# Kernel optimization log

Hardware: AMD Instinct MI355X
Metric: run time of the kernel (lower is better)

The kernel has to match this reference:

```python
import jax, jax.numpy as jnp
import numpy as np
import math

T, N, D, H = 1024, 8, 1024, 16
HD = D // H  # head_dim = 64


def setup_inputs() -> dict:
    key = jax.random.key(0)
    k1, k2, k3, k4 = jax.random.split(key, 4)
    scale = 1.0 / math.sqrt(D)  # roughly xavier-scale params
    return {
        "x": jax.random.normal(k1, (T, N, D), dtype=jnp.float32),
        "q_weight": jax.random.normal(k2, (D, H, HD), dtype=jnp.float32) * scale,
        "v_weight": jax.random.normal(k3, (D, H, HD), dtype=jnp.float32) * scale,
        "out_w": jax.random.normal(k4, (D, D), dtype=jnp.float32) * scale,
        "out_b": jnp.zeros((D,), dtype=jnp.float32),
    }


def reference(x, q_weight, v_weight, out_w, out_b):
    inv_sqrt_hd = 1.0 / math.sqrt(HD)
    # q = k : (T, N, H, HD)
    q = jnp.einsum('tbm,mhd->tbhd', x, q_weight)
    q_sq = jnp.einsum('tbhd,tbhd->tbh', q, q)  # squared norms
    # squared L2 distance logits: (T, S, N, H)
    squared_dist = q_sq[:, None] + q_sq[None, :] - 2.0 * jnp.einsum('tbhd,sbhd->tsbh', q, q)
    attn_logits = -squared_dist * inv_sqrt_hd
    attn_weights = jax.nn.softmax(attn_logits, axis=1)  # softmax over source dim S
    # A = W_q W_q^T per head: (H, D, D)
    A = jnp.einsum('mhd,nhd->hmn', q_weight, q_weight) * inv_sqrt_hd
    XA = jnp.einsum('tbm,hmn->tbhn', x, A)           # (T, N, H, D)
    PXA = jnp.einsum('tsbh,sbhm->tbhm', attn_weights, XA)  # (T, N, H, D)
    PXAV = jnp.einsum('tbhm,mhd->tbhd', PXA, v_weight).reshape(T, N, D)
    return PXAV @ out_w.T + out_b
```

## Files before the change

### kernel.cpp

```cpp
#include <hip/hip_runtime.h>
#include <hip/hip_bf16.h>

#define T_ 1024
#define N_ 8
#define D_ 1024
#define H_ 16
#define HD_ 64

typedef __attribute__((ext_vector_type(8))) short bf16x8;
typedef __attribute__((ext_vector_type(4))) float f32x4;
typedef __attribute__((ext_vector_type(16))) float f32x16;
typedef __attribute__((ext_vector_type(4))) int i32x4;
typedef __attribute__((ext_vector_type(2))) int i32x2;
typedef unsigned short u16;
typedef unsigned int u32;

__device__ __forceinline__ float bf2f(u16 u){
  union { float f; unsigned int i; } v; v.i = ((unsigned int)u) << 16; return v.f;
}
__device__ __forceinline__ u16 f2bf(float f){
  union { float f; unsigned int i; } v; v.f = f;
  unsigned int r = v.i + 0x7FFFu + ((v.i >> 16) & 1u);
  return (u16)(r >> 16);
}
__device__ __forceinline__ u16 f2bf_fast(float f){
  __hip_bfloat16 h = __float2bfloat16(f);
  return *reinterpret_cast<u16*>(&h);
}
__device__ __forceinline__ float exp2_raw(float x){
  float r;
  asm("v_exp_f32 %0, %1" : "=v"(r) : "v"(x));
  return r;
}

__global__ __launch_bounds__(256) void k_wqt(const float* __restrict__ Wq, u16* __restrict__ Wqt){
  __shared__ float tld[64][65];
  int m0 = blockIdx.x * 64, n0 = blockIdx.y * 64;
  int col = threadIdx.x & 63, rq = threadIdx.x >> 6;
  #pragma unroll
  for (int p = 0; p < 16; ++p){
    int row = rq * 16 + p;
    tld[row][col] = Wq[(size_t)(m0 + row) * D_ + n0 + col];
  }
  __syncthreads();
  #pragma unroll
  for (int p = 0; p < 16; ++p){
    int row = rq * 16 + p;
    Wqt[(size_t)(n0 + row) * D_ + m0 + col] = f2bf(tld[col][row]);
  }
}

__global__ __launch_bounds__(256) void k_bmatp(const float* __restrict__ qw, const float* __restrict__ vw,
                                               float* __restrict__ Bp){
  int h = (int)blockIdx.x >> 3, sp = (int)blockIdx.x & 7;
  int tid = threadIdx.x, lane = tid & 63, w = tid >> 6;
  int g = lane >> 4, c = lane & 15;
  __shared__ u16 Qt[64 * 72];
  __shared__ u16 Vt[64 * 72];
  f32x4 zero = {0.f, 0.f, 0.f, 0.f};
  f32x4 acc[4];
  #pragma unroll
  for (int eb = 0; eb < 4; ++eb) acc[eb] = zero;
  int m = tid >> 2, cg = tid & 3;
  for (int mt = sp * 128; mt < sp * 128 + 128; mt += 64){
    __syncthreads();
    #pragma unroll
    for (int q = 0; q < 4; ++q){
      int e0 = cg * 16 + q * 4;
      f32x4 vq = *(const f32x4*)(qw + (size_t)(mt + m) * D_ + h * 64 + e0);
      f32x4 vv = *(const f32x4*)(vw + (size_t)(mt + m) * D_ + h * 64 + e0);
      #pragma unroll
      for (int j = 0; j < 4; ++j){
        Qt[(e0 + j) * 72 + m] = f2bf_fast(vq[j]);
        Vt[(e0 + j) * 72 + m] = f2bf_fast(vv[j]);
      }
    }
    __syncthreads();
    #pragma unroll
    for (int kk = 0; kk < 2; ++kk){
      bf16x8 av = *(const bf16x8*)&Vt[(w * 16 + c) * 72 + kk * 32 + g * 8];
      #pragma unroll
      for (int eb = 0; eb < 4; ++eb){
        bf16x8 bq = *(const bf16x8*)&Qt[(eb * 16 + c) * 72 + kk * 32 + g * 8];
        acc[eb] = __builtin_amdgcn_mfma_f32_16x16x32_bf16(av, bq, acc[eb], 0, 0, 0);
      }
    }
  }
  #pragma unroll
  for (int eb = 0; eb < 4; ++eb)
    #pragma unroll
    for (int r = 0; r < 4; ++r){
      int d = w * 16 + g * 4 + r, e = eb * 16 + c;
      Bp[(((size_t)sp * 16 + h) * 64 + d) * 64 + e] = acc[eb][r];
    }
}

__global__ __launch_bounds__(256) void k_bred(const float* __restrict__ Bp, u16* __restrict__ Bt){
  int i = blockIdx.x * 256 + threadIdx.x;
  float s = 0.f;
  #pragma unroll
  for (int j = 0; j < 8; ++j) s += Bp[(size_t)j * 65536 + i];
  Bt[i] = f2bf(s * 0.125f);
}

__device__ __forceinline__ int swz(int row, int colbyte){
  return row * 64 + (((colbyte) ^ ((row & 7) << 4)) >> 1);
}

template<int A_F32, int B_F32, int EPI>
__global__ __launch_bounds__(256) void k_gemm(const void* __restrict__ A_, const void* __restrict__ B_,
                                              void* __restrict__ Cv, const float* __restrict__ bias,
                                              int M, int N, int K){
  int nbn = N >> 7;
  int ii = (int)blockIdx.x;
  int sw = (ii & 7) * 64 + (ii >> 3);
  int bm = sw / nbn, bn = sw % nbn;
  int tid = threadIdx.x, lane = tid & 63, wid = tid >> 6;
  int wr = wid >> 1, wc = wid & 1, g = lane >> 4, c = lane & 15;
  __shared__ u16 As[128 * 64];
  __shared__ u16 Bs[128 * 64];
  f32x4 zero = {0.f, 0.f, 0.f, 0.f};
  f32x4 acc[4][4];
  #pragma unroll
  for (int m = 0; m < 4; ++m)
    #pragma unroll
    for (int n = 0; n < 4; ++n) acc[m][n] = zero;
  for (int kt = 0; kt < K; kt += 64){
    __syncthreads();
    #pragma unroll
    for (int p = 0; p < 4; ++p){
      int ci = tid + p * 256;
      int row = ci >> 3, c8 = ci & 7;
      int dst = swz(row, c8 * 16);
      if (A_F32){
        const float* A = (const float*)A_;
        const float* src = A + (size_t)(bm * 128 + row) * K + kt + c8 * 8;
        f32x4 v0 = *(const f32x4*)src;
        f32x4 v1 = *(const f32x4*)(src + 4);
        union { u16 u[8]; i32x4 v; } pk;
        #pragma unroll
        for (int j = 0; j < 4; ++j){ pk.u[j] = f2bf_fast(v0[j]); pk.u[4 + j] = f2bf_fast(v1[j]); }
        *(i32x4*)&As[dst] = pk.v;
      } else {
        const u16* A = (const u16*)A_;
        *(i32x4*)&As[dst] = *(const i32x4*)(A + (size_t)(bm * 128 + row) * K + kt + c8 * 8);
      }
      if (B_F32){
        const float* B = (const float*)B_;
        const float* src = B + (size_t)(bn * 128 + row) * K + kt + c8 * 8;
        f32x4 v0 = *(const f32x4*)src;
        f32x4 v1 = *(const f32x4*)(src + 4);
        union { u16 u[8]; i32x4 v; } pk;
        #pragma unroll
        for (int j = 0; j < 4; ++j){ pk.u[j] = f2bf_fast(v0[j]); pk.u[4 + j] = f2bf_fast(v1[j]); }
        *(i32x4*)&Bs[dst] = pk.v;
      } else {
        const u16* B = (const u16*)B_;
        *(i32x4*)&Bs[dst] = *(const i32x4*)(B + (size_t)(bn * 128 + row) * K + kt + c8 * 8);
      }
    }
    __syncthreads();
    #pragma unroll
    for (int kk = 0; kk < 2; ++kk){
      bf16x8 af[4], bfr[4];
      #pragma unroll
      for (int m = 0; m < 4; ++m){
        int row = wr * 64 + m * 16 + c;
        af[m] = *(const bf16x8*)&As[swz(row, kk * 64 + g * 16)];
      }
      #pragma unroll
      for (int n = 0; n < 4; ++n){
        int row = wc * 64 + n * 16 + c;
        bfr[n] = *(const bf16x8*)&Bs[swz(row, kk * 64 + g * 16)];
      }
      #pragma unroll
      for (int m = 0; m < 4; ++m)
        #pragma unroll
        for (int n = 0; n < 4; ++n)
          acc[m][n] = __builtin_amdgcn_mfma_f32_16x16x32_bf16(af[m], bfr[n], acc[m][n], 0, 0, 0);
    }
  }
  #pragma unroll
  for (int m = 0; m < 4; ++m)
    #pragma unroll
    for (int n = 0; n < 4; ++n)
      #pragma unroll
      for (int r = 0; r < 4; ++r){
        int row = bm * 128 + wr * 64 + m * 16 + g * 4 + r;
        int col = bn * 128 + wc * 64 + n * 16 + c;
        float v = acc[m][n][r];
        if (EPI == 0){
          int t = row >> 3, b = row & 7, hh = col >> 6, dd = col & 63;
          ((u16*)Cv)[(((size_t)(b * H_ + hh)) * T_ + t) * HD_ + dd] = f2bf(v);
        } else {
          ((float*)Cv)[(size_t)row * N + col] = v + bias[col];
        }
      }
}

__global__ __launch_bounds__(64) void k_u(const u16* __restrict__ qb, const u16* __restrict__ Bt,
                                          u16* __restrict__ ubt, float* __restrict__ qsq){
  int bh = blockIdx.x >> 4, tt = blockIdx.x & 15;
  int h = bh & 15, t0 = tt * 64;
  int lane = threadIdx.x, g = lane >> 4, c = lane & 15;
  const float QS_SCALE = 0.125f * 1.44269504088896340736f;
  bf16x8 af[4][2], bq[4][2];
  #pragma unroll
  for (int mf = 0; mf < 4; ++mf)
    #pragma unroll
    for (int kk = 0; kk < 2; ++kk)
      af[mf][kk] = *(const bf16x8*)(Bt + ((size_t)(h * 64 + mf * 16 + c)) * 64 + kk * 32 + g * 8);
  #pragma unroll
  for (int nf = 0; nf < 4; ++nf)
    #pragma unroll
    for (int kk = 0; kk < 2; ++kk)
      bq[nf][kk] = *(const bf16x8*)(qb + ((size_t)(bh * 1024 + t0 + nf * 16 + c)) * 64 + kk * 32 + g * 8);
  #pragma unroll
  for (int nf = 0; nf < 4; ++nf){
    float ss = 0.f;
    #pragma unroll
    for (int kk = 0; kk < 2; ++kk)
      #pragma unroll
      for (int j = 0; j < 8; ++j){ float f = bf2f((u16)bq[nf][kk][j]); ss = fmaf(f, f, ss); }
    ss += __shfl_xor(ss, 16);
    ss += __shfl_xor(ss, 32);
    if (lane < 16) qsq[(size_t)bh * 1024 + t0 + nf * 16 + lane] = ss * QS_SCALE;
  }
  f32x4 zero = {0.f, 0.f, 0.f, 0.f};
  f32x4 acc[4][4];
  #pragma unroll
  for (int mf = 0; mf < 4; ++mf)
    #pragma unroll
    for (int nf = 0; nf < 4; ++nf) acc[mf][nf] = zero;
  #pragma unroll
  for (int kk = 0; kk < 2; ++kk)
    #pragma unroll
    for (int mf = 0; mf < 4; ++mf)
      #pragma unroll
      for (int nf = 0; nf < 4; ++nf)
        acc[mf][nf] = __builtin_amdgcn_mfma_f32_16x16x32_bf16(af[mf][kk], bq[nf][kk], acc[mf][nf], 0, 0, 0);
  #pragma unroll
  for (int mf = 0; mf < 4; ++mf)
    #pragma unroll
    for (int nf = 0; nf < 4; ++nf)
      #pragma unroll
      for (int r = 0; r < 4; ++r)
        ubt[((size_t)(bh * 64 + mf * 16 + g * 4 + r)) * 1024 + t0 + nf * 16 + c] = f2bf(acc[mf][nf][r]);
}

__global__ __launch_bounds__(256) void k_attn(const u16* __restrict__ qb, const u16* __restrict__ ubt,
                                              const float* __restrict__ qsq, u16* __restrict__ obm){
  int i = (int)blockIdx.x;
  int bh = ((i & 7) << 4) + (i >> 6);
  int tt = (i >> 3) & 7;
  int b = bh >> 4, h = bh & 15;
  int tid = threadIdx.x, w = tid >> 6, lane = tid & 63;
  int lo = lane & 31, hi = lane >> 5;
  __shared__ u16 Kl[64 * 64];
  __shared__ u16 Ul[64 * 64];
  const float C1 = 0.25f * 1.44269504088896340736f;
  int t0 = tt * 128 + w * 32;
  const u16* qbh = qb + (size_t)bh * 65536;
  const u16* ubh = ubt + (size_t)bh * 65536;
  const float* qsb = qsq + (size_t)bh * 1024;
  bf16x8 qB[4];
  #pragma unroll
  for (int kd = 0; kd < 4; ++kd)
    qB[kd] = *(const bf16x8*)(qbh + (t0 + lo) * 64 + kd * 16 + hi * 8);
  f32x16 o0 = {0,0,0,0,0,0,0,0,0,0,0,0,0,0,0,0};
  f32x16 o1 = {0,0,0,0,0,0,0,0,0,0,0,0,0,0,0,0};
  float l_c = 0.f;
  int srow = tid >> 3, sc8 = tid & 7;
  int srow2 = (tid + 256) >> 3, sc82 = tid & 7;
  int sdst1 = swz(srow, sc8 * 16), sdst2 = swz(srow2, sc82 * 16);
  i32x4 rK[2], rU[2];
  rK[0] = *(const i32x4*)(qbh + srow * 64 + sc8 * 8);
  rK[1] = *(const i32x4*)(qbh + srow2 * 64 + sc82 * 8);
  rU[0] = *(const i32x4*)(ubh + (size_t)srow * 1024 + sc8 * 8);
  rU[1] = *(const i32x4*)(ubh + (size_t)srow2 * 1024 + sc82 * 8);
  for (int st = 0; st < 16; ++st){
    int s0 = st * 64;
    if (st) __syncthreads();
    *(i32x4*)&Kl[sdst1] = rK[0];
    *(i32x4*)&Kl[sdst2] = rK[1];
    *(i32x4*)&Ul[sdst1] = rU[0];
    *(i32x4*)&Ul[sdst2] = rU[1];
    if (st < 15){
      int s1 = s0 + 64;
      rK[0] = *(const i32x4*)(qbh + (s1 + srow) * 64 + sc8 * 8);
      rK[1] = *(const i32x4*)(qbh + (s1 + srow2) * 64 + sc82 * 8);
      rU[0] = *(const i32x4*)(ubh + (size_t)srow * 1024 + s1 + sc8 * 8);
      rU[1] = *(const i32x4*)(ubh + (size_t)srow2 * 1024 + s1 + sc82 * 8);
    }
    __syncthreads();
    u32 W[16];
    #pragma unroll
    for (int ts = 0; ts < 2; ++ts){
      int sb = ts * 32;
      f32x16 sf = {0,0,0,0,0,0,0,0,0,0,0,0,0,0,0,0};
      __builtin_amdgcn_s_setprio(1);
      #pragma unroll
      for (int kd = 0; kd < 4; ++kd){
        bf16x8 kA = *(const bf16x8*)&Kl[swz(sb + lo, kd * 32 + hi * 16)];
        sf = __builtin_amdgcn_mfma_f32_32x32x16_bf16(kA, qB[kd], sf, 0, 0, 0);
      }
      __builtin_amdgcn_s_setprio(0);
      f32x4 qs[4];
      #pragma unroll
      for (int q = 0; q < 4; ++q)
        qs[q] = *(const f32x4*)(qsb + s0 + sb + q * 8 + hi * 4);
      float p[16];
      #pragma unroll
      for (int r = 0; r < 16; ++r)
        p[r] = exp2_raw(fmaf(sf[r], C1, -qs[r >> 2][r & 3]));
      float sA = ((p[0] + p[1]) + (p[2] + p[3])) + ((p[4] + p[5]) + (p[6] + p[7]));
      float sB = ((p[8] + p[9]) + (p[10] + p[11])) + ((p[12] + p[13]) + (p[14] + p[15]));
      l_c += sA + sB;
      #pragma unroll
      for (int q = 0; q < 8; ++q)
        W[ts * 8 + q] = ((u32)f2bf_fast(p[2 * q + 1]) << 16) | (u32)f2bf_fast(p[2 * q]);
    }
    #pragma unroll
    for (int m = 0; m < 4; ++m){
      int base = (m >> 1) * 8 + (m & 1) * 4;
      i32x2 sw0 = __builtin_amdgcn_permlane32_swap((int)W[base + 0], (int)W[base + 2], false, false);
      i32x2 sw1 = __builtin_amdgcn_permlane32_swap((int)W[base + 1], (int)W[base + 3], false, false);
      union { u32 wd[4]; bf16x8 v; } pa;
      pa.wd[0] = (u32)sw0[0]; pa.wd[1] = (u32)sw1[0]; pa.wd[2] = (u32)sw0[1]; pa.wd[3] = (u32)sw1[1];
      bf16x8 u0 = *(const bf16x8*)&Ul[swz(lo, m * 32 + hi * 16)];
      bf16x8 u1 = *(const bf16x8*)&Ul[swz(32 + lo, m * 32 + hi * 16)];
      __builtin_amdgcn_s_setprio(1);
      o0 = __builtin_amdgcn_mfma_f32_32x32x16_bf16(pa.v, u0, o0, 0, 0, 0);
      o1 = __builtin_amdgcn_mfma_f32_32x32x16_bf16(pa.v, u1, o1, 0, 0, 0);
      __builtin_amdgcn_s_setprio(0);
    }
  }
  l_c += __shfl_xor(l_c, 32);
  float inv = 1.0f / l_c;
  #pragma unroll
  for (int r = 0; r < 16; ++r){
    int tr = (r & 3) + 8 * (r >> 2) + 4 * hi;
    float invr = __shfl(inv, tr);
    size_t rowb = ((size_t)((t0 + tr) * 8 + b)) * 1024 + h * 64;
    obm[rowb + lo] = f2bf(o0[r] * invr);
    obm[rowb + 32 + lo] = f2bf(o1[r] * invr);
  }
}

extern "C" void kernel_launch(void* const* d_in, const int* in_sizes, int n_in,
                              void* d_out, int out_size, void* d_ws, size_t ws_size,
                              hipStream_t stream) {
  const float* x   = (const float*)d_in[0];
  const float* qw  = (const float*)d_in[1];
  const float* vw  = (const float*)d_in[2];
  const float* ow  = (const float*)d_in[3];
  const float* ob_bias = (const float*)d_in[4];
  float* out = (float*)d_out;

  float* Bp = (float*)d_out;
  u16* qb  = (u16*)d_out;
  u16* ubt = (u16*)((char*)d_out + (size_t)16 * 1024 * 1024);

  char* ws = (char*)d_ws;
  size_t off = 0;
  auto alloc = [&](size_t bytes) -> void* {
    void* p = ws + off;
    off += (bytes + 255) & ~(size_t)255;
    return p;
  };
  u16*   wqt = (u16*)  alloc((size_t)1024 * 1024 * 2);
  u16*   obm = (u16*)  alloc((size_t)8192 * 1024 * 2);
  float* qsq = (float*)alloc((size_t)128 * 1024 * 4);
  u16*   Bt  = (u16*)  alloc((size_t)16 * 64 * 64 * 2);

  k_bmatp<<<128, 256, 0, stream>>>(qw, vw, Bp);
  k_bred<<<256, 256, 0, stream>>>(Bp, Bt);
  k_wqt<<<dim3(16, 16), 256, 0, stream>>>(qw, wqt);
  k_gemm<1, 0, 0><<<512, 256, 0, stream>>>(x, wqt, qb, nullptr, 8192, 1024, 1024);
  k_u<<<2048, 64, 0, stream>>>(qb, Bt, ubt, qsq);
  k_attn<<<1024, 256, 0, stream>>>(qb, ubt, qsq, obm);
  k_gemm<0, 1, 1><<<512, 256, 0, stream>>>(obm, ow, out, ob_bias, 8192, 1024, 1024);
}
```

Before: 140.9 us.

## Load attention K/U tiles directly into LDS and interleave PV per half-tile

The register-staged prefetch of K and U tiles is replaced with global_load_lds direct-to-LDS copies, using a pre-swizzled source column so the LDS layout matches the existing swz pattern. The per-tile squared norms are also staged through LDS. The PV MFMAs now run inside each 32-row half instead of after both halves, and occupancy is hinted at 4 blocks per CU. This is meant to cut VGPR pressure and LDS-store instructions, at the cost of losing the previous overlap where the next tile was fetched during compute, since the loads now sit between two barriers.

```diff
diff --git a/kernel.cpp b/kernel.cpp
--- a/kernel.cpp
+++ b/kernel.cpp
@@ -31,6 +31,18 @@
   float r;
   asm("v_exp_f32 %0, %1" : "=v"(r) : "v"(x));
   return r;
+}
+__device__ __forceinline__ void gl_lds16(const u16* g, u16* l){
+  __builtin_amdgcn_global_load_lds(
+      (const __attribute__((address_space(1))) unsigned int*)g,
+      (__attribute__((address_space(3))) unsigned int*)(unsigned int)(unsigned long long)l,
+      16, 0, 0);
+}
+__device__ __forceinline__ void gl_lds4(const float* g, float* l){
+  __builtin_amdgcn_global_load_lds(
+      (const __attribute__((address_space(1))) unsigned int*)g,
+      (__attribute__((address_space(3))) unsigned int*)(unsigned int)(unsigned long long)l,
+      4, 0, 0);
 }
 
 __global__ __launch_bounds__(256) void k_wqt(const float* __restrict__ Wq, u16* __restrict__ Wqt){
@@ -248,8 +260,8 @@
         ubt[((size_t)(bh * 64 + mf * 16 + g * 4 + r)) * 1024 + t0 + nf * 16 + c] = f2bf(acc[mf][nf][r]);
 }
 
-__global__ __launch_bounds__(256) void k_attn(const u16* __restrict__ qb, const u16* __restrict__ ubt,
-                                              const float* __restrict__ qsq, u16* __restrict__ obm){
+__global__ __launch_bounds__(256, 4) void k_attn(const u16* __restrict__ qb, const u16* __restrict__ ubt,
+                                                 const float* __restrict__ qsq, u16* __restrict__ obm){
   int i = (int)blockIdx.x;
   int bh = ((i & 7) << 4) + (i >> 6);
   int tt = (i >> 3) & 7;
@@ -258,6 +270,7 @@
   int lo = lane & 31, hi = lane >> 5;
   __shared__ u16 Kl[64 * 64];
   __shared__ u16 Ul[64 * 64];
+  __shared__ float Qs[64];
   const float C1 = 0.25f * 1.44269504088896340736f;
   int t0 = tt * 128 + w * 32;
   const u16* qbh = qb + (size_t)bh * 65536;
@@ -269,70 +282,64 @@
     qB[kd] = *(const bf16x8*)(qbh + (t0 + lo) * 64 + kd * 16 + hi * 8);
   f32x16 o0 = {0,0,0,0,0,0,0,0,0,0,0,0,0,0,0,0};
   f32x16 o1 = {0,0,0,0,0,0,0,0,0,0,0,0,0,0,0,0};
+  const f32x16 zero16 = {0,0,0,0,0,0,0,0,0,0,0,0,0,0,0,0};
   float l_c = 0.f;
-  int srow = tid >> 3, sc8 = tid & 7;
-  int srow2 = (tid + 256) >> 3, sc82 = tid & 7;
-  int sdst1 = swz(srow, sc8 * 16), sdst2 = swz(srow2, sc82 * 16);
-  i32x4 rK[2], rU[2];
-  rK[0] = *(const i32x4*)(qbh + srow * 64 + sc8 * 8);
-  rK[1] = *(const i32x4*)(qbh + srow2 * 64 + sc82 * 8);
-  rU[0] = *(const i32x4*)(ubh + (size_t)srow * 1024 + sc8 * 8);
-  rU[1] = *(const i32x4*)(ubh + (size_t)srow2 * 1024 + sc82 * 8);
+  int slot0 = (w * 2 + 0) * 64 + lane, slot1 = (w * 2 + 1) * 64 + lane;
+  int r0 = slot0 >> 3, sc0 = ((slot0 & 7) ^ (r0 & 7)) * 8;
+  int r1 = slot1 >> 3, sc1 = ((slot1 & 7) ^ (r1 & 7)) * 8;
+  u16* kD0 = &Kl[(w * 2 + 0) * 512];
+  u16* kD1 = &Kl[(w * 2 + 1) * 512];
+  u16* uD0 = &Ul[(w * 2 + 0) * 512];
+  u16* uD1 = &Ul[(w * 2 + 1) * 512];
   for (int st = 0; st < 16; ++st){
     int s0 = st * 64;
-    if (st) __syncthreads();
-    *(i32x4*)&Kl[sdst1] = rK[0];
-    *(i32x4*)&Kl[sdst2] = rK[1];
-    *(i32x4*)&Ul[sdst1] = rU[0];
-    *(i32x4*)&Ul[sdst2] = rU[1];
-    if (st < 15){
-      int s1 = s0 + 64;
-      rK[0] = *(const i32x4*)(qbh + (s1 + srow) * 64 + sc8 * 8);
-      rK[1] = *(const i32x4*)(qbh + (s1 + srow2) * 64 + sc82 * 8);
-      rU[0] = *(const i32x4*)(ubh + (size_t)srow * 1024 + s1 + sc8 * 8);
-      rU[1] = *(const i32x4*)(ubh + (size_t)srow2 * 1024 + s1 + sc82 * 8);
-    }
-    __syncthreads();
-    u32 W[16];
+    __syncthreads();
+    gl_lds16(qbh + (s0 + r0) * 64 + sc0, kD0);
+    gl_lds16(qbh + (s0 + r1) * 64 + sc1, kD1);
+    gl_lds16(ubh + (size_t)r0 * 1024 + s0 + sc0, uD0);
+    gl_lds16(ubh + (size_t)r1 * 1024 + s0 + sc1, uD1);
+    if (w == 0) gl_lds4(qsb + s0 + lane, &Qs[0]);
+    __syncthreads();
     #pragma unroll
     for (int ts = 0; ts < 2; ++ts){
-      int sb = ts * 32;
-      f32x16 sf = {0,0,0,0,0,0,0,0,0,0,0,0,0,0,0,0};
+      f32x16 sf = zero16;
       __builtin_amdgcn_s_setprio(1);
       #pragma unroll
       for (int kd = 0; kd < 4; ++kd){
-        bf16x8 kA = *(const bf16x8*)&Kl[swz(sb + lo, kd * 32 + hi * 16)];
+        bf16x8 kA = *(const bf16x8*)&Kl[swz(ts * 32 + lo, kd * 32 + hi * 16)];
         sf = __builtin_amdgcn_mfma_f32_32x32x16_bf16(kA, qB[kd], sf, 0, 0, 0);
       }
       __builtin_amdgcn_s_setprio(0);
-      f32x4 qs[4];
+      f32x4 qs_[4];
       #pragma unroll
       for (int q = 0; q < 4; ++q)
-        qs[q] = *(const f32x4*)(qsb + s0 + sb + q * 8 + hi * 4);
+        qs_[q] = *(const f32x4*)&Qs[ts * 32 + q * 8 + hi * 4];
       float p[16];
       #pragma unroll
       for (int r = 0; r < 16; ++r)
-        p[r] = exp2_raw(fmaf(sf[r], C1, -qs[r >> 2][r & 3]));
+        p[r] = exp2_raw(fmaf(sf[r], C1, -qs_[r >> 2][r & 3]));
       float sA = ((p[0] + p[1]) + (p[2] + p[3])) + ((p[4] + p[5]) + (p[6] + p[7]));
       float sB = ((p[8] + p[9]) + (p[10] + p[11])) + ((p[12] + p[13]) + (p[14] + p[15]));
       l_c += sA + sB;
+      u32 W[8];
       #pragma unroll
       for (int q = 0; q < 8; ++q)
-        W[ts * 8 + q] = ((u32)f2bf_fast(p[2 * q + 1]) << 16) | (u32)f2bf_fast(p[2 * q]);
-    }
-    #pragma unroll
-    for (int m = 0; m < 4; ++m){
-      int base = (m >> 1) * 8 + (m & 1) * 4;
-      i32x2 sw0 = __builtin_amdgcn_permlane32_swap((int)W[base + 0], (int)W[base + 2], false, false);
-      i32x2 sw1 = __builtin_amdgcn_permlane32_swap((int)W[base + 1], (int)W[base + 3], false, false);
-      union { u32 wd[4]; bf16x8 v; } pa;
-      pa.wd[0] = (u32)sw0[0]; pa.wd[1] = (u32)sw1[0]; pa.wd[2] = (u32)sw0[1]; pa.wd[3] = (u32)sw1[1];
-      bf16x8 u0 = *(const bf16x8*)&Ul[swz(lo, m * 32 + hi * 16)];
-      bf16x8 u1 = *(const bf16x8*)&Ul[swz(32 + lo, m * 32 + hi * 16)];
-      __builtin_amdgcn_s_setprio(1);
-      o0 = __builtin_amdgcn_mfma_f32_32x32x16_bf16(pa.v, u0, o0, 0, 0, 0);
-      o1 = __builtin_amdgcn_mfma_f32_32x32x16_bf16(pa.v, u1, o1, 0, 0, 0);
-      __builtin_amdgcn_s_setprio(0);
+        W[q] = ((u32)f2bf_fast(p[2 * q + 1]) << 16) | (u32)f2bf_fast(p[2 * q]);
+      #pragma unroll
+      for (int ml = 0; ml < 2; ++ml){
+        int m_g = ts * 2 + ml;
+        int base = ml * 4;
+        i32x2 sw0 = __builtin_amdgcn_permlane32_swap((int)W[base + 0], (int)W[base + 2], false, false);
+        i32x2 sw1 = __builtin_amdgcn_permlane32_swap((int)W[base + 1], (int)W[base + 3], false, false);
+        union { u32 wd[4]; bf16x8 v; } pa;
+        pa.wd[0] = (u32)sw0[0]; pa.wd[1] = (u32)sw1[0]; pa.wd[2] = (u32)sw0[1]; pa.wd[3] = (u32)sw1[1];
+        bf16x8 u0 = *(const bf16x8*)&Ul[swz(lo, m_g * 32 + hi * 16)];
+        bf16x8 u1 = *(const bf16x8*)&Ul[swz(32 + lo, m_g * 32 + hi * 16)];
+        __builtin_amdgcn_s_setprio(1);
+        o0 = __builtin_amdgcn_mfma_f32_32x32x16_bf16(pa.v, u0, o0, 0, 0, 0);
+        o1 = __builtin_amdgcn_mfma_f32_32x32x16_bf16(pa.v, u1, o1, 0, 0, 0);
+        __builtin_amdgcn_s_setprio(0);
+      }
     }
   }
   l_c += __shfl_xor(l_c, 32);
```

Result: no change. 141.8 us (+0.7%).
